# Kernel optimization log

Measured on AMD Instinct MI355X. Metric: run time of the kernel, lower is better.

Reference implementation:

```python
import jax, jax.numpy as jnp
import numpy as np

B = 32768      # batch of ODE state evaluations
N = 64         # input_size (number of variables / per-node MLPs)
H = 64         # hidden_size
N_DISCRETE = 16  # first 16 variables use straight-through gating
HIDDEN_FLAG = True


def setup_inputs() -> dict:
    key = jax.random.key(0)
    k1, k2, k3 = jax.random.split(key, 3)
    inputs = jax.random.normal(k1, (B, N), jnp.float32)
    # Stacked per-node MLP weights: net_i is Linear(N,H,bias=False) -> ReLU -> Linear(H,1,bias=False)
    W1 = jax.random.normal(k2, (N, H, N), jnp.float32) / np.sqrt(N).astype(np.float32)
    W2 = jax.random.normal(k3, (N, H), jnp.float32) / np.sqrt(H).astype(np.float32)
    adjacency = jnp.ones((N, N), jnp.float32)  # buffer, initialized to ones
    discrete_mask = jnp.arange(N) < N_DISCRETE  # bool [N], from input_type_list
    return {"t": 0, "inputs": inputs, "W1": W1, "W2": W2,
            "adjacency": adjacency, "discrete_mask": discrete_mask}


def reference(t, inputs, W1, W2, adjacency, discrete_mask):
    # Straight-through discrete gating: y_hard - sg(y_soft) + y_soft
    y_soft = jax.nn.sigmoid(inputs)
    st = (inputs > 0).astype(inputs.dtype) - jax.lax.stop_gradient(y_soft) + y_soft
    x = jnp.where(discrete_mask[None, :], st, inputs)  # [B, N]

    # Effective per-node input mask: row i of adjacency; last node additionally
    # filtered to only its own (hidden) feature when hidden_flag is set.
    M = adjacency
    if HIDDEN_FLAG:
        one_hot_last = jnp.zeros((N,), M.dtype).at[-1].set(1.0)
        M = M.at[-1].set(M[-1] * one_hot_last)

    # Masking the input of node i by M[i] is equivalent to masking W1[i]'s input dim.
    W1m = W1 * M[:, None, :]                      # [N, H, N]
    h = jax.nn.relu(jnp.einsum('bn,ihn->bih', x, W1m))  # [B, N, H]
    out = jnp.einsum('bih,ih->bi', h, W2)               # [B, N]
    return out
```

## Files before the change

kernel.cpp:

```cpp
#include <hip/hip_runtime.h>
#include <stdint.h>


typedef __attribute__((ext_vector_type(8))) short short8;
typedef __attribute__((ext_vector_type(4))) float floatx4;

#define NN 64
#define HH 64
#define BB 32768
#define OTW 33
#define X_ELEMS (BB * NN)
#define W1_ELEMS (NN * HH * NN)

__device__ __forceinline__ unsigned short f32_to_bf16_bits(float f) {
    union { float f; unsigned int i; } c; c.f = f;
    unsigned int b = c.i;
    b += 0x7fffu + ((b >> 16) & 1u);
    return (unsigned short)(b >> 16);
}

__device__ __forceinline__ bool sniff_bf16(const void* x) {
    const int lane = threadIdx.x & 63;
    const ushort* xw = (const ushort*)x;
    const ushort a = xw[4 * lane];
    const ushort b = xw[4 * lane + 2];
    const int ea = (a >> 7) & 0xFF, eb = (b >> 7) & 0xFF;
    const int hit = ((ea >= 118 && ea <= 132) ? 1 : 0) + ((eb >= 118 && eb <= 132) ? 1 : 0);
    const unsigned long long m1 = __ballot(hit >= 1);
    const unsigned long long m2 = __ballot(hit >= 2);
    return (__popcll(m1) + __popcll(m2)) >= 64;
}

__global__ __launch_bounds__(256, 4)
void prep_kernel(const void* __restrict__ x, const void* __restrict__ w1,
                 ushort* __restrict__ xo, ushort* __restrict__ w1o)
{
    const bool is_bf16 = sniff_bf16(x);
    const long base = ((long)blockIdx.x * 256 + (long)threadIdx.x) * 8;

    if (base < X_ELEMS) {
        const bool gate = (base & 63) < 16;
        short8 v;
        if (is_bf16) {
            v = *(const short8*)((const ushort*)x + base);
            if (gate) {
                #pragma unroll
                for (int j = 0; j < 8; ++j) {
                    const unsigned short u = (unsigned short)v[j];
                    const bool pos = ((u & 0x8000u) == 0) && ((u & 0x7fffu) != 0);
                    v[j] = pos ? (short)0x3F80 : (short)0;
                }
            }
        } else {
            const float* p = (const float*)x + base;
            const float4 f0 = *(const float4*)(p);
            const float4 f1 = *(const float4*)(p + 4);
            const float vals[8] = {f0.x, f0.y, f0.z, f0.w, f1.x, f1.y, f1.z, f1.w};
            #pragma unroll
            for (int j = 0; j < 8; ++j) {
                if (gate) v[j] = (vals[j] > 0.f) ? (short)0x3F80 : (short)0;
                else      v[j] = (short)f32_to_bf16_bits(vals[j]);
            }
        }
        *(short8*)(xo + base) = v;
    } else {
        const long wb = base - X_ELEMS;
        if (wb < W1_ELEMS) {
            short8 v;
            if (is_bf16) {
                v = *(const short8*)((const ushort*)w1 + wb);
            } else {
                const float* p = (const float*)w1 + wb;
                const float4 f0 = *(const float4*)(p);
                const float4 f1 = *(const float4*)(p + 4);
                const float vals[8] = {f0.x, f0.y, f0.z, f0.w, f1.x, f1.y, f1.z, f1.w};
                #pragma unroll
                for (int j = 0; j < 8; ++j) v[j] = (short)f32_to_bf16_bits(vals[j]);
            }
            const int node = (int)(wb >> 12);
            if (node == NN - 1) {
                const int w63 = (int)(wb & 63);
                #pragma unroll
                for (int j = 0; j < 8; ++j)
                    if (w63 + j != NN - 1) v[j] = 0;
            }
            *(short8*)(w1o + wb) = v;
        }
    }
}

template<bool F32>
__device__ __forceinline__ void main_body(const ushort* __restrict__ xo,
                                          const ushort* __restrict__ w1o,
                                          const void* __restrict__ w2p,
                                          void* __restrict__ outp,
                                          float* outTile)
{
    const int tid  = threadIdx.x;
    const int wave = tid >> 6;
    const int lane = tid & 63;
    const int quad = lane >> 4;
    const int l16  = lane & 15;

    const int blk   = blockIdx.x;
    const int b0    = (blk >> 1) * 64;
    const int nhalf = blk & 1;
    const int nbase = nhalf * 32 + wave * 8;

    short8 xfrag[2][4];
    #pragma unroll
    for (int ks = 0; ks < 2; ++ks)
        #pragma unroll
        for (int nt = 0; nt < 4; ++nt)
            xfrag[ks][nt] = *(const short8*)(xo + (b0 + nt * 16 + l16) * NN + ks * 32 + quad * 8);

    auto loadW1 = [&](short8 w[2][4], int node) {
        const ushort* w1n = w1o + node * (HH * NN);
        #pragma unroll
        for (int ks = 0; ks < 2; ++ks)
            #pragma unroll
            for (int mt = 0; mt < 4; ++mt)
                w[ks][mt] = *(const short8*)(w1n + (mt * 16 + l16) * NN + ks * 32 + quad * 8);
    };

    auto computeNode = [&](const short8 w[2][4], int node) {
        float w2v[4][4];
        #pragma unroll
        for (int mt = 0; mt < 4; ++mt) {
            const int idx = node * HH + mt * 16 + quad * 4;
            if (F32) {
                const float4 ww = *(const float4*)((const float*)w2p + idx);
                w2v[mt][0] = ww.x; w2v[mt][1] = ww.y; w2v[mt][2] = ww.z; w2v[mt][3] = ww.w;
            } else {
                const ushort4 ww = *(const ushort4*)((const ushort*)w2p + idx);
                union { unsigned int i; float f; } c0, c1, c2, c3;
                c0.i = ((unsigned int)ww.x) << 16; c1.i = ((unsigned int)ww.y) << 16;
                c2.i = ((unsigned int)ww.z) << 16; c3.i = ((unsigned int)ww.w) << 16;
                w2v[mt][0] = c0.f; w2v[mt][1] = c1.f; w2v[mt][2] = c2.f; w2v[mt][3] = c3.f;
            }
        }

        floatx4 acc[4][4];
        #pragma unroll
        for (int mt = 0; mt < 4; ++mt)
            #pragma unroll
            for (int nt = 0; nt < 4; ++nt)
                acc[mt][nt] = (floatx4){0.f, 0.f, 0.f, 0.f};

        #pragma unroll
        for (int ks = 0; ks < 2; ++ks)
            #pragma unroll
            for (int mt = 0; mt < 4; ++mt)
                #pragma unroll
                for (int nt = 0; nt < 4; ++nt)
                    acc[mt][nt] = __builtin_amdgcn_mfma_f32_16x16x32_bf16(
                        w[ks][mt], xfrag[ks][nt], acc[mt][nt], 0, 0, 0);

        float psum[4];
        #pragma unroll
        for (int nt = 0; nt < 4; ++nt) {
            float s0 = 0.f, s1 = 0.f;
            #pragma unroll
            for (int mt = 0; mt < 4; ++mt) {
                float a0 = acc[mt][nt][0]; a0 = a0 > 0.f ? a0 : 0.f;
                float a1 = acc[mt][nt][1]; a1 = a1 > 0.f ? a1 : 0.f;
                float a2 = acc[mt][nt][2]; a2 = a2 > 0.f ? a2 : 0.f;
                float a3 = acc[mt][nt][3]; a3 = a3 > 0.f ? a3 : 0.f;
                s0 = fmaf(a0, w2v[mt][0], s0); s1 = fmaf(a1, w2v[mt][1], s1);
                s0 = fmaf(a2, w2v[mt][2], s0); s1 = fmaf(a3, w2v[mt][3], s1);
            }
            psum[nt] = s0 + s1;
        }

        #pragma unroll
        for (int nt = 0; nt < 4; ++nt) {
            psum[nt] += __shfl_xor(psum[nt], 16, 64);
            psum[nt] += __shfl_xor(psum[nt], 32, 64);
        }

        const float val = (quad == 0) ? psum[0] : (quad == 1) ? psum[1]
                         : (quad == 2) ? psum[2] : psum[3];
        outTile[lane * OTW + (node & 31)] = val;
    };

    short8 wA[2][4], wB[2][4];
    loadW1(wA, nbase);
    #pragma unroll 1
    for (int np = 0; np < 8; np += 2) {
        loadW1(wB, nbase + np + 1);
        computeNode(wA, nbase + np);
        if (np + 2 < 8) loadW1(wA, nbase + np + 2);
        computeNode(wB, nbase + np + 1);
    }

    __syncthreads();

    const int row = tid >> 2;
    const int q   = tid & 3;
    const float* rp = outTile + row * OTW + q * 8;
    const size_t obase = (size_t)(b0 + row) * NN + nhalf * 32 + q * 8;
    if (F32) {
        float* op = (float*)outp + obase;
        *(float4*)(op)     = make_float4(rp[0], rp[1], rp[2], rp[3]);
        *(float4*)(op + 4) = make_float4(rp[4], rp[5], rp[6], rp[7]);
    } else {
        ushort* op = (ushort*)outp + obase;
        short8 o;
        #pragma unroll
        for (int c = 0; c < 8; ++c) o[c] = (short)f32_to_bf16_bits(rp[c]);
        *(short8*)(op) = o;
    }
}

__global__ __launch_bounds__(256, 2)
void main_kernel(const void* __restrict__ xorig,
                 const ushort* __restrict__ xo, const ushort* __restrict__ w1o,
                 const void* __restrict__ w2p, void* __restrict__ outp)
{
    __shared__ float outTile[64 * OTW];
    const bool is_bf16 = sniff_bf16(xorig);
    if (is_bf16) main_body<false>(xo, w1o, w2p, outp, outTile);
    else         main_body<true >(xo, w1o, w2p, outp, outTile);
}

#define LDSW 20
template<bool F32>
__device__ __forceinline__ void run_body_fb(const void* xp, const void* w1p,
                                            const void* w2p, void* outp,
                                            float* myLds)
{
    const int tid  = threadIdx.x;
    const int wave = tid >> 6;
    const int lane = tid & 63;
    const int quad = lane >> 4;
    const int l16  = lane & 15;
    const int blk  = blockIdx.x;
    const int ng   = blk >> 7;
    const int rbg  = blk & 127;
    const int node = ng * 4 + wave;
    const int rowbase = rbg * 256;

    short8 bfrag[2][4];
    #pragma unroll
    for (int ks = 0; ks < 2; ++ks) {
        #pragma unroll
        for (int ht = 0; ht < 4; ++ht) {
            const int h = ht * 16 + l16;
            const int k = ks * 32 + quad * 8;
            short8 v;
            if (F32) {
                const float* p = (const float*)w1p + node * (HH * NN) + h * NN + k;
                const float4 a0 = *(const float4*)(p);
                const float4 a1 = *(const float4*)(p + 4);
                const float vals[8] = {a0.x, a0.y, a0.z, a0.w, a1.x, a1.y, a1.z, a1.w};
                #pragma unroll
                for (int j = 0; j < 8; ++j) v[j] = (short)f32_to_bf16_bits(vals[j]);
            } else {
                v = *(const short8*)((const ushort*)w1p + node * (HH * NN) + h * NN + k);
            }
            if (node == NN - 1) {
                #pragma unroll
                for (int j = 0; j < 8; ++j)
                    if (k + j != NN - 1) v[j] = 0;
            }
            bfrag[ks][ht] = v;
        }
    }

    float w2reg[4];
    #pragma unroll
    for (int ht = 0; ht < 4; ++ht) {
        const int idx = node * HH + ht * 16 + l16;
        if (F32) {
            w2reg[ht] = ((const float*)w2p)[idx];
        } else {
            const ushort u = ((const ushort*)w2p)[idx];
            union { unsigned int i; float f; } cv; cv.i = ((unsigned int)u) << 16;
            w2reg[ht] = cv.f;
        }
    }

    #pragma unroll 1
    for (int it = 0; it < 4; ++it) {
        const int b0 = rowbase + it * 64;
        short8 afrag[2][4];
        #pragma unroll
        for (int ks = 0; ks < 2; ++ks) {
            #pragma unroll
            for (int rt = 0; rt < 4; ++rt) {
                const int rowg = b0 + rt * 16 + l16;
                const int k    = ks * 32 + quad * 8;
                const bool gate = (ks == 0 && quad < 2);
                short8 v;
                if (F32) {
                    const float* p = (const float*)xp + rowg * NN + k;
                    const float4 a0 = *(const float4*)(p);
                    const float4 a1 = *(const float4*)(p + 4);
                    const float vals[8] = {a0.x, a0.y, a0.z, a0.w, a1.x, a1.y, a1.z, a1.w};
                    #pragma unroll
                    for (int j = 0; j < 8; ++j) {
                        if (gate) v[j] = (vals[j] > 0.f) ? (short)0x3F80 : (short)0;
                        else      v[j] = (short)f32_to_bf16_bits(vals[j]);
                    }
                } else {
                    v = *(const short8*)((const ushort*)xp + rowg * NN + k);
                    if (gate) {
                        #pragma unroll
                        for (int j = 0; j < 8; ++j) {
                            const unsigned short u = (unsigned short)v[j];
                            const bool pos = ((u & 0x8000u) == 0) && ((u & 0x7fffu) != 0);
                            v[j] = pos ? (short)0x3F80 : (short)0;
                        }
                    }
                }
                afrag[ks][rt] = v;
            }
        }

        floatx4 acc[4][4];
        #pragma unroll
        for (int rt = 0; rt < 4; ++rt)
            #pragma unroll
            for (int ht = 0; ht < 4; ++ht)
                acc[rt][ht] = (floatx4){0.f, 0.f, 0.f, 0.f};
        #pragma unroll
        for (int ks = 0; ks < 2; ++ks)
            #pragma unroll
            for (int rt = 0; rt < 4; ++rt)
                #pragma unroll
                for (int ht = 0; ht < 4; ++ht)
                    acc[rt][ht] = __builtin_amdgcn_mfma_f32_16x16x32_bf16(
                        afrag[ks][rt], bfrag[ks][ht], acc[rt][ht], 0, 0, 0);

        #pragma unroll
        for (int rt = 0; rt < 4; ++rt) {
            #pragma unroll
            for (int r = 0; r < 4; ++r) {
                float s = 0.f;
                #pragma unroll
                for (int ht = 0; ht < 4; ++ht) {
                    float v = acc[rt][ht][r];
                    v = v > 0.f ? v : 0.f;
                    s = fmaf(v, w2reg[ht], s);
                }
                myLds[(rt * 16 + quad * 4 + r) * LDSW + l16] = s;
            }
        }
        __syncthreads();
        const float* rowp = myLds + lane * LDSW;
        const float4 v0 = *(const float4*)(rowp + 0);
        const float4 v1 = *(const float4*)(rowp + 4);
        const float4 v2 = *(const float4*)(rowp + 8);
        const float4 v3 = *(const float4*)(rowp + 12);
        const float tot = (((v0.x + v0.y) + (v0.z + v0.w)) + ((v1.x + v1.y) + (v1.z + v1.w)))
                        + (((v2.x + v2.y) + (v2.z + v2.w)) + ((v3.x + v3.y) + (v3.z + v3.w)));
        if (F32) ((float*) outp)[(size_t)(b0 + lane) * NN + node] = tot;
        else     ((ushort*)outp)[(size_t)(b0 + lane) * NN + node] = f32_to_bf16_bits(tot);
        __syncthreads();
    }
}

__global__ __launch_bounds__(256, 2)
void fallback_kernel(const void* __restrict__ x, const void* __restrict__ W1,
                     const void* __restrict__ W2, void* __restrict__ out)
{
    __shared__ float lds[4][64 * LDSW];
    const bool is_bf16 = sniff_bf16(x);
    float* myLds = &lds[threadIdx.x >> 6][0];
    if (is_bf16) run_body_fb<false>(x, W1, W2, out, myLds);
    else         run_body_fb<true >(x, W1, W2, out, myLds);
}

extern "C" void kernel_launch(void* const* d_in, const int* in_sizes, int n_in,
                              void* d_out, int out_size, void* d_ws, size_t ws_size,
                              hipStream_t stream) {
    int i_in = -1, i_w1 = -1, i_w2 = -1;
    for (int i = 0; i < n_in; ++i) {
        const int s = in_sizes[i];
        if      (s == BB * NN  && i_in < 0) i_in = i;
        else if (s == NN*HH*NN && i_w1 < 0) i_w1 = i;
        else if (s == NN*HH    && i_w2 < 0) i_w2 = i;
    }
    if (i_in < 0) i_in = (n_in > 1) ? 1 : 0;
    if (i_w1 < 0) i_w1 = i_in + 1;
    if (i_w2 < 0) i_w2 = i_w1 + 1;

    const size_t need = (size_t)(X_ELEMS + W1_ELEMS) * sizeof(ushort);
    if (ws_size >= need) {
        ushort* xo  = (ushort*)d_ws;
        ushort* w1o = xo + X_ELEMS;
        prep_kernel<<<dim3((X_ELEMS + W1_ELEMS) / (256 * 8)), dim3(256), 0, stream>>>(
            d_in[i_in], d_in[i_w1], xo, w1o);
        main_kernel<<<dim3(1024), dim3(256), 0, stream>>>(
            d_in[i_in], xo, w1o, d_in[i_w2], d_out);
    } else {
        fallback_kernel<<<dim3(16 * 128), dim3(256), 0, stream>>>(
            d_in[i_in], d_in[i_w1], d_in[i_w2], d_out);
    }
}
```

Before: 115.6 us.

## Stream W1 per m-tile with single buffer and raise occupancy bound

Replaces the double-buffered whole-node W1 fragments with a single buffer refilled one m-tile at a time, right after that tile's MFMAs finish. ReLU and the W2 reduction are folded in per m-tile, so only four accumulators are live instead of sixteen. Together with launch_bounds raised from 2 to 4 blocks per SIMD, this is meant to cut register pressure and raise occupancy so more waves hide memory latency. The cost is less prefetch distance per load, which risks exposing load latency within each node.

```diff
diff --git a/kernel.cpp b/kernel.cpp
--- a/kernel.cpp
+++ b/kernel.cpp
@@ -114,16 +114,21 @@
         for (int nt = 0; nt < 4; ++nt)
             xfrag[ks][nt] = *(const short8*)(xo + (b0 + nt * 16 + l16) * NN + ks * 32 + quad * 8);
 
-    auto loadW1 = [&](short8 w[2][4], int node) {
-        const ushort* w1n = w1o + node * (HH * NN);
-        #pragma unroll
-        for (int ks = 0; ks < 2; ++ks)
-            #pragma unroll
-            for (int mt = 0; mt < 4; ++mt)
-                w[ks][mt] = *(const short8*)(w1n + (mt * 16 + l16) * NN + ks * 32 + quad * 8);
+    short8 w[2][4];
+    auto loadW1mt = [&](int node, int mt) {
+        const ushort* w1n = w1o + node * (HH * NN) + (mt * 16 + l16) * NN + quad * 8;
+        w[0][mt] = *(const short8*)(w1n);
+        w[1][mt] = *(const short8*)(w1n + 32);
     };
 
-    auto computeNode = [&](const short8 w[2][4], int node) {
+    #pragma unroll
+    for (int mt = 0; mt < 4; ++mt) loadW1mt(nbase, mt);
+
+    #pragma unroll 1
+    for (int np = 0; np < 8; ++np) {
+        const int node = nbase + np;
+        const int nextnode = (np < 7) ? (node + 1) : node;
+
         float w2v[4][4];
         #pragma unroll
         for (int mt = 0; mt < 4; ++mt) {
@@ -140,36 +145,34 @@
             }
         }
 
-        floatx4 acc[4][4];
-        #pragma unroll
-        for (int mt = 0; mt < 4; ++mt)
-            #pragma unroll
-            for (int nt = 0; nt < 4; ++nt)
-                acc[mt][nt] = (floatx4){0.f, 0.f, 0.f, 0.f};
-
-        #pragma unroll
-        for (int ks = 0; ks < 2; ++ks)
-            #pragma unroll
-            for (int mt = 0; mt < 4; ++mt)
+        float psum[4] = {0.f, 0.f, 0.f, 0.f};
+
+        #pragma unroll
+        for (int mt = 0; mt < 4; ++mt) {
+            floatx4 acc[4];
+            #pragma unroll
+            for (int nt = 0; nt < 4; ++nt) acc[nt] = (floatx4){0.f, 0.f, 0.f, 0.f};
+            #pragma unroll
+            for (int ks = 0; ks < 2; ++ks)
                 #pragma unroll
                 for (int nt = 0; nt < 4; ++nt)
-                    acc[mt][nt] = __builtin_amdgcn_mfma_f32_16x16x32_bf16(
-                        w[ks][mt], xfrag[ks][nt], acc[mt][nt], 0, 0, 0);
-
-        float psum[4];
-        #pragma unroll
-        for (int nt = 0; nt < 4; ++nt) {
-            float s0 = 0.f, s1 = 0.f;
-            #pragma unroll
-            for (int mt = 0; mt < 4; ++mt) {
-                float a0 = acc[mt][nt][0]; a0 = a0 > 0.f ? a0 : 0.f;
-                float a1 = acc[mt][nt][1]; a1 = a1 > 0.f ? a1 : 0.f;
-                float a2 = acc[mt][nt][2]; a2 = a2 > 0.f ? a2 : 0.f;
-                float a3 = acc[mt][nt][3]; a3 = a3 > 0.f ? a3 : 0.f;
-                s0 = fmaf(a0, w2v[mt][0], s0); s1 = fmaf(a1, w2v[mt][1], s1);
-                s0 = fmaf(a2, w2v[mt][2], s0); s1 = fmaf(a3, w2v[mt][3], s1);
-            }
-            psum[nt] = s0 + s1;
+                    acc[nt] = __builtin_amdgcn_mfma_f32_16x16x32_bf16(
+                        w[ks][mt], xfrag[ks][nt], acc[nt], 0, 0, 0);
+
+            loadW1mt(nextnode, mt);
+
+            #pragma unroll
+            for (int nt = 0; nt < 4; ++nt) {
+                float a0 = acc[nt][0]; a0 = a0 > 0.f ? a0 : 0.f;
+                float a1 = acc[nt][1]; a1 = a1 > 0.f ? a1 : 0.f;
+                float a2 = acc[nt][2]; a2 = a2 > 0.f ? a2 : 0.f;
+                float a3 = acc[nt][3]; a3 = a3 > 0.f ? a3 : 0.f;
+                float s0 = fmaf(a0, w2v[mt][0], psum[nt]);
+                float s1 = a1 * w2v[mt][1];
+                s0 = fmaf(a2, w2v[mt][2], s0);
+                s1 = fmaf(a3, w2v[mt][3], s1);
+                psum[nt] = s0 + s1;
+            }
         }
 
         #pragma unroll
@@ -181,16 +184,6 @@
         const float val = (quad == 0) ? psum[0] : (quad == 1) ? psum[1]
                          : (quad == 2) ? psum[2] : psum[3];
         outTile[lane * OTW + (node & 31)] = val;
-    };
-
-    short8 wA[2][4], wB[2][4];
-    loadW1(wA, nbase);
-    #pragma unroll 1
-    for (int np = 0; np < 8; np += 2) {
-        loadW1(wB, nbase + np + 1);
-        computeNode(wA, nbase + np);
-        if (np + 2 < 8) loadW1(wA, nbase + np + 2);
-        computeNode(wB, nbase + np + 1);
     }
 
     __syncthreads();
@@ -212,7 +205,7 @@
     }
 }
 
-__global__ __launch_bounds__(256, 2)
+__global__ __launch_bounds__(256, 4)
 void main_kernel(const void* __restrict__ xorig,
                  const ushort* __restrict__ xo, const ushort* __restrict__ w1o,
                  const void* __restrict__ w2p, void* __restrict__ outp)
```

Result: no change. 113.8 us (-1.5%).
